# Kernel tuning notes

Hardware: AMD Instinct MI355X
Metric: run time of the kernel (lower is better)

## Reference

```python
import jax, jax.numpy as jnp
import numpy as np

N_NODES = 100000
N_EDGES = 1000000
IN_FEATS = 128


def setup_inputs() -> dict:
    key = jax.random.key(0)
    k_h, k_src, k_dst, k_w = jax.random.split(key, 4)
    h = jax.random.normal(k_h, (N_NODES, IN_FEATS), dtype=jnp.float32)
    src_idx = jax.random.randint(k_src, (N_EDGES,), 0, N_NODES, dtype=jnp.int32)
    dst_idx = jax.random.randint(k_dst, (N_EDGES,), 0, N_NODES, dtype=jnp.int32)
    # torch nn.Linear(2*in_feats, 1): weight [1, 2*in_feats], bias [1]
    bound = 1.0 / np.sqrt(2 * IN_FEATS)
    W = jax.random.uniform(k_w, (1, 2 * IN_FEATS), dtype=jnp.float32, minval=-bound, maxval=bound)
    b = jnp.zeros((1,), dtype=jnp.float32)
    return {"h": h, "src_idx": src_idx, "dst_idx": dst_idx, "W": W, "b": b}


def reference(h, src_idx, dst_idx, W, b):
    # gather per-edge src/dst node features: [E, D] each
    x = jnp.concatenate([h[src_idx], h[dst_idx]], axis=1)  # [E, 2D]
    score = x @ W.T + b                                     # [E, 1]
    return score
```

## Files before the change

### kernel.cpp

```cpp
#include <hip/hip_runtime.h>

#define IN_FEATS 128

__global__ void __launch_bounds__(256)
node_partial_kernel(const float* __restrict__ h,
                    const float* __restrict__ W,
                    const float* __restrict__ bptr,
                    float* __restrict__ s_src,
                    float* __restrict__ s_dst,
                    int n_nodes) {
    int tid  = threadIdx.x;
    int grp  = tid >> 4;
    int l16  = tid & 15;
    int node = blockIdx.x * 16 + grp;
    if (node >= n_nodes) return;

    const float4* hp = (const float4*)(h + (size_t)node * IN_FEATS);
    const float4* Wsরp = (const float4*)W;
    const float4* Wdp = (const float4*)(W + IN_FEATS);

    float4 x0  = hp[l16];
    float4 x1  = hp[l16 + 16];
    float4 ws0 = Wsরp[l16];
    float4 ws1 = Wsরp[l16 + 16];
    float4 wd0 = Wdp[l16];
    float4 wd1 = Wdp[l16 + 16];

    float ps = x0.x * ws0.x + x0.y * ws0.y + x0.z * ws0.z + x0.w * ws0.w
             + x1.x * ws1.x + x1.y * ws1.y + x1.z * ws1.z + x1.w * ws1.w;
    float pd = x0.x * wd0.x + x0.y * wd0.y + x0.z * wd0.z + x0.w * wd0.w
             + x1.x * wd1.x + x1.y * wd1.y + x1.z * wd1.z + x1.w * wd1.w;

    #pragma unroll
    for (int m = 8; m > 0; m >>= 1) {
        ps += __shfl_xor(ps, m, 64);
        pd += __shfl_xor(pd, m, 64);
    }
    if (l16 == 0) {
        s_src[node] = ps + bptr[0];
        s_dst[node] = pd;
    }
}

__global__ void __launch_bounds__(256)
edge_score_kernel(const int* __restrict__ src_idx,
                  const int* __restrict__ dst_idx,
                  const float* __restrict__ s_src,
                  const float* __restrict__ s_dst,
                  float* __restrict__ out,
                  int n_edges) {
    int i8   = blockIdx.x * blockDim.x + threadIdx.x;
    int base = i8 * 8;
    if (base + 7 < n_edges) {
        int4 s0 = ((const int4*)src_idx)[i8 * 2];
        int4 s1 = ((const int4*)src_idx)[i8 * 2 + 1];
        int4 d0 = ((const int4*)dst_idx)[i8 * 2];
        int4 d1 = ((const int4*)dst_idx)[i8 * 2 + 1];
        float4 o0, o1;
        o0.x = s_src[s0.x] + s_dst[d0.x];
        o0.y = s_src[s0.y] + s_dst[d0.y];
        o0.z = s_src[s0.z] + s_dst[d0.z];
        o0.w = s_src[s0.w] + s_dst[d0.w];
        o1.x = s_src[s1.x] + s_dst[d1.x];
        o1.y = s_src[s1.y] + s_dst[d1.y];
        o1.z = s_src[s1.z] + s_dst[d1.z];
        o1.w = s_src[s1.w] + s_dst[d1.w];
        ((float4*)out)[i8 * 2]     = o0;
        ((float4*)out)[i8 * 2 + 1] = o1;
    } else if (base < n_edges) {
        for (int e = base; e < n_edges; ++e)
            out[e] = s_src[src_idx[e]] + s_dst[dst_idx[e]];
    }
}

__global__ void __launch_bounds__(256)
edge_direct_kernel(const float* __restrict__ h,
                   const int* __restrict__ src_idx,
                   const int* __restrict__ dst_idx,
                   const float* __restrict__ W,
                   const float* __restrict__ bptr,
                   float* __restrict__ out,
                   int n_edges) {
    int e = blockIdx.x * blockDim.x + threadIdx.x;
    if (e >= n_edges) return;
    const float4* hs = (const float4*)(h + (size_t)src_idx[e] * IN_FEATS);
    const float4* hd = (const float4*)(h + (size_t)dst_idx[e] * IN_FEATS);
    const float4* Ws = (const float4*)W;
    const float4* Wd = (const float4*)(W + IN_FEATS);
    float acc = bptr[0];
    #pragma unroll
    for (int k = 0; k < IN_FEATS / 4; ++k) {
        float4 a = hs[k], w = Ws[k];
        acc += a.x * w.x + a.y * w.y + a.z * w.z + a.w * w.w;
        float4 c = hd[k], u = Wd[k];
        acc += c.x * u.x + c.y * u.y + c.z * u.z + c.w * u.w;
    }
    out[e] = acc;
}

extern "C" void kernel_launch(void* const* d_in, const int* in_sizes, int n_in,
                              void* d_out, int out_size, void* d_ws, size_t ws_size,
                              hipStream_t stream) {
    const float* h       = (const float*)d_in[0];
    const int*   src_idx = (const int*)d_in[1];
    const int*   dst_idx = (const int*)d_in[2];
    const float* W       = (const float*)d_in[3];
    const float* b       = (const float*)d_in[4];
    float*       out     = (float*)d_out;

    const int n_nodes = in_sizes[0] / IN_FEATS;
    const int n_edges = in_sizes[1];

    const size_t ws_needed = 2 * (size_t)n_nodes * sizeof(float);

    if (ws_size >= ws_needed) {
        float* s_src = (float*)d_ws;
        float* s_dst = s_src + n_nodes;

        int grid1 = (n_nodes + 15) / 16;
        node_partial_kernel<<<grid1, 256, 0, stream>>>(h, W, b, s_src, s_dst,
                                                       n_nodes);

        int n_groups = (n_edges + 7) / 8;
        int grid2 = (n_groups + 255) / 256;
        edge_score_kernel<<<grid2, 256, 0, stream>>>(src_idx, dst_idx, s_src,
                                                     s_dst, out, n_edges);
    } else {
        int grid = (n_edges + 255) / 256;
        edge_direct_kernel<<<grid, 256, 0, stream>>>(h, src_idx, dst_idx, W, b,
                                                     out, n_edges);
    }
}
```

Before: 100.8 us.

## Fuse node and edge phases into one cooperative kernel with grid sync

Merges the node-partial and edge-score kernels into a single cooperative launch of 1024 blocks that uses a grid-wide sync between the phases, prefetching edge indices before the node phase. The per-node scores are interleaved into a float2 array so each gather touches one buffer, and the node phase now uses 8 lanes per node with 4 float4 loads each. This removes one kernel launch and the gap between the kernels, at the cost of grid-sync overhead and a persistent grid-stride schedule that may underfill the device. A fallback path with two kernels remains if the cooperative launch fails.

```diff
diff --git a/kernel.cpp b/kernel.cpp
--- a/kernel.cpp
+++ b/kernel.cpp
@@ -1,76 +1,121 @@
 #include <hip/hip_runtime.h>
+#include <hip/hip_cooperative_groups.h>
+
+namespace cg = cooperative_groups;
 
 #define IN_FEATS 128
+
+__device__ __forceinline__ float dot4(float4 a, float4 b) {
+    return a.x * b.x + a.y * b.y + a.z * b.z + a.w * b.w;
+}
+
+__device__ __forceinline__ void node_phase(const float* __restrict__ h,
+                                           const float* __restrict__ W,
+                                           float bias,
+                                           float2* __restrict__ s,
+                                           int n_nodes,
+                                           int block_base,
+                                           int grid_stride) {
+    const int tid = threadIdx.x;
+    const int grp = tid >> 3;
+    const int l8  = tid & 7;
+
+    const float4* Ws4 = (const float4*)W;
+    const float4* Wd4 = Ws4 + (IN_FEATS / 4);
+    const float4 ws0 = Ws4[l8],      ws1 = Ws4[l8 + 8],
+                 ws2 = Ws4[l8 + 16], ws3 = Ws4[l8 + 24];
+    const float4 wd0 = Wd4[l8],      wd1 = Wd4[l8 + 8],
+                 wd2 = Wd4[l8 + 16], wd3 = Wd4[l8 + 24];
+
+    for (int node = block_base + grp; node < n_nodes; node += grid_stride) {
+        const float4* hp = (const float4*)(h + (size_t)node * IN_FEATS);
+        float4 x0 = hp[l8];
+        float4 x1 = hp[l8 + 8];
+        float4 x2 = hp[l8 + 16];
+        float4 x3 = hp[l8 + 24];
+        float ps = dot4(x0, ws0) + dot4(x1, ws1) + dot4(x2, ws2) + dot4(x3, ws3);
+        float pd = dot4(x0, wd0) + dot4(x1, wd1) + dot4(x2, wd2) + dot4(x3, wd3);
+        #pragma unroll
+        for (int m = 4; m > 0; m >>= 1) {
+            ps += __shfl_xor(ps, m, 64);
+            pd += __shfl_xor(pd, m, 64);
+        }
+        if (l8 == 0) s[node] = make_float2(ps + bias, pd);
+    }
+}
+
+__global__ void __launch_bounds__(256, 4)
+fused_kernel(const float* __restrict__ h,
+             const int* __restrict__ src_idx,
+             const int* __restrict__ dst_idx,
+             const float* __restrict__ W,
+             const float* __restrict__ bptr,
+             float2* __restrict__ s,
+             float* __restrict__ out,
+             int n_nodes, int n_edges) {
+    const int gsz  = gridDim.x * blockDim.x;
+    const int gtid = blockIdx.x * blockDim.x + threadIdx.x;
+    const int n_g4 = n_edges >> 2;
+
+    int4 pf_s = make_int4(0, 0, 0, 0), pf_d = make_int4(0, 0, 0, 0);
+    if (gtid < n_g4) {
+        pf_s = ((const int4*)src_idx)[gtid];
+        pf_d = ((const int4*)dst_idx)[gtid];
+    }
+
+    node_phase(h, W, bptr[0], s, n_nodes, blockIdx.x * 32, gridDim.x * 32);
+
+    __threadfence();
+    cg::this_grid().sync();
+    __threadfence();
+
+    for (int g = gtid; g < n_g4; g += gsz) {
+        int4 a = pf_s, c = pf_d;
+        if (g != gtid) {
+            a = ((const int4*)src_idx)[g];
+            c = ((const int4*)dst_idx)[g];
+        }
+        float4 o;
+        o.x = s[a.x].x + s[c.x].y;
+        o.y = s[a.y].x + s[c.y].y;
+        o.z = s[a.z].x + s[c.z].y;
+        o.w = s[a.w].x + s[c.w].y;
+        ((float4*)out)[g] = o;
+    }
+    for (int e = (n_g4 << 2) + gtid; e < n_edges; e += gsz)
+        out[e] = s[src_idx[e]].x + s[dst_idx[e]].y;
+}
 
 __global__ void __launch_bounds__(256)
 node_partial_kernel(const float* __restrict__ h,
                     const float* __restrict__ W,
                     const float* __restrict__ bptr,
-                    float* __restrict__ s_src,
-                    float* __restrict__ s_dst,
+                    float2* __restrict__ s,
                     int n_nodes) {
-    int tid  = threadIdx.x;
-    int grp  = tid >> 4;
-    int l16  = tid & 15;
-    int node = blockIdx.x * 16 + grp;
-    if (node >= n_nodes) return;
-
-    const float4* hp = (const float4*)(h + (size_t)node * IN_FEATS);
-    const float4* Wsরp = (const float4*)W;
-    const float4* Wdp = (const float4*)(W + IN_FEATS);
-
-    float4 x0  = hp[l16];
-    float4 x1  = hp[l16 + 16];
-    float4 ws0 = Wsরp[l16];
-    float4 ws1 = Wsরp[l16 + 16];
-    float4 wd0 = Wdp[l16];
-    float4 wd1 = Wdp[l16 + 16];
-
-    float ps = x0.x * ws0.x + x0.y * ws0.y + x0.z * ws0.z + x0.w * ws0.w
-             + x1.x * ws1.x + x1.y * ws1.y + x1.z * ws1.z + x1.w * ws1.w;
-    float pd = x0.x * wd0.x + x0.y * wd0.y + x0.z * wd0.z + x0.w * wd0.w
-             + x1.x * wd1.x + x1.y * wd1.y + x1.z * wd1.z + x1.w * wd1.w;
-
-    #pragma unroll
-    for (int m = 8; m > 0; m >>= 1) {
-        ps += __shfl_xor(ps, m, 64);
-        pd += __shfl_xor(pd, m, 64);
-    }
-    if (l16 == 0) {
-        s_src[node] = ps + bptr[0];
-        s_dst[node] = pd;
-    }
+    node_phase(h, W, bptr[0], s, n_nodes, blockIdx.x * 32, gridDim.x * 32);
 }
 
 __global__ void __launch_bounds__(256)
 edge_score_kernel(const int* __restrict__ src_idx,
                   const int* __restrict__ dst_idx,
-                  const float* __restrict__ s_src,
-                  const float* __restrict__ s_dst,
+                  const float2* __restrict__ s,
                   float* __restrict__ out,
                   int n_edges) {
-    int i8   = blockIdx.x * blockDim.x + threadIdx.x;
-    int base = i8 * 8;
-    if (base + 7 < n_edges) {
-        int4 s0 = ((const int4*)src_idx)[i8 * 2];
-        int4 s1 = ((const int4*)src_idx)[i8 * 2 + 1];
-        int4 d0 = ((const int4*)dst_idx)[i8 * 2];
-        int4 d1 = ((const int4*)dst_idx)[i8 * 2 + 1];
-        float4 o0, o1;
-        o0.x = s_src[s0.x] + s_dst[d0.x];
-        o0.y = s_src[s0.y] + s_dst[d0.y];
-        o0.z = s_src[s0.z] + s_dst[d0.z];
-        o0.w = s_src[s0.w] + s_dst[d0.w];
-        o1.x = s_src[s1.x] + s_dst[d1.x];
-        o1.y = s_src[s1.y] + s_dst[d1.y];
-        o1.z = s_src[s1.z] + s_dst[d1.z];
-        o1.w = s_src[s1.w] + s_dst[d1.w];
-        ((float4*)out)[i8 * 2]     = o0;
-        ((float4*)out)[i8 * 2 + 1] = o1;
-    } else if (base < n_edges) {
-        for (int e = base; e < n_edges; ++e)
-            out[e] = s_src[src_idx[e]] + s_dst[dst_idx[e]];
+    const int gsz  = gridDim.x * blockDim.x;
+    const int gtid = blockIdx.x * blockDim.x + threadIdx.x;
+    const int n_g4 = n_edges >> 2;
+    for (int g = gtid; g < n_g4; g += gsz) {
+        int4 a = ((const int4*)src_idx)[g];
+        int4 c = ((const int4*)dst_idx)[g];
+        float4 o;
+        o.x = s[a.x].x + s[c.x].y;
+        o.y = s[a.y].x + s[c.y].y;
+        o.z = s[a.z].x + s[c.z].y;
+        o.w = s[a.w].x + s[c.w].y;
+        ((float4*)out)[g] = o;
     }
+    for (int e = (n_g4 << 2) + gtid; e < n_edges; e += gsz)
+        out[e] = s[src_idx[e]].x + s[dst_idx[e]].y;
 }
 
 __global__ void __launch_bounds__(256)
@@ -111,20 +156,27 @@
     const int n_nodes = in_sizes[0] / IN_FEATS;
     const int n_edges = in_sizes[1];
 
-    const size_t ws_needed = 2 * (size_t)n_nodes * sizeof(float);
+    const size_t ws_needed = (size_t)n_nodes * sizeof(float2);
 
     if (ws_size >= ws_needed) {
-        float* s_src = (float*)d_ws;
-        float* s_dst = s_src + n_nodes;
+        float2* s = (float2*)d_ws;
 
-        int grid1 = (n_nodes + 15) / 16;
-        node_partial_kernel<<<grid1, 256, 0, stream>>>(h, W, b, s_src, s_dst,
-                                                       n_nodes);
+        void* args[] = { (void*)&h, (void*)&src_idx, (void*)&dst_idx,
+                         (void*)&W, (void*)&b, (void*)&s, (void*)&out,
+                         (void*)&n_nodes, (void*)&n_edges };
+        hipError_t err = hipLaunchCooperativeKernel(
+            reinterpret_cast<void*>(fused_kernel),
+            dim3(1024), dim3(256), args, 0, stream);
 
-        int n_groups = (n_edges + 7) / 8;
-        int grid2 = (n_groups + 255) / 256;
-        edge_score_kernel<<<grid2, 256, 0, stream>>>(src_idx, dst_idx, s_src,
-                                                     s_dst, out, n_edges);
+        if (err != hipSuccess) {
+            int g1 = (n_nodes + 31) / 32;
+            node_partial_kernel<<<g1, 256, 0, stream>>>(h, W, b, s, n_nodes);
+            int n_g4 = n_edges >> 2;
+            int g2 = (n_g4 + 255) / 256;
+            if (g2 < 1) g2 = 1;
+            edge_score_kernel<<<g2, 256, 0, stream>>>(src_idx, dst_idx, s, out,
+                                                      n_edges);
+        }
     } else {
         int grid = (n_edges + 255) / 256;
         edge_direct_kernel<<<grid, 256, 0, stream>>>(h, src_idx, dst_idx, W, b,
```

Measured after the change: 358.8 us. +256.0%, slower.
